# Performance work log

Hardware: AMD Instinct MI355X
Metric: run time of the kernel (lower is better)

## Reference

```python
import jax, jax.numpy as jnp
import numpy as np

B, S_IMG, S_TXT, H, D = 1, 2048, 512, 24, 128
HID = H * D  # 3072
S_TOT = S_TXT + S_IMG
IP_SCALE = 1.0
EPS = 1e-5


def setup_inputs() -> dict:
    key = jax.random.key(0)
    ks = jax.random.split(key, 16)
    r = lambda k, s: jax.random.normal(k, s, dtype=jnp.float32)
    w = lambda k, s: r(k, s) * 0.02
    theta = r(ks[15], (S_TOT, D))  # rotary angles over joint sequence
    z = lambda: jnp.zeros((HID,), jnp.float32)
    return dict(
        hidden_states=r(ks[0], (B, S_IMG, HID)),
        encoder_hidden_states=r(ks[1], (B, S_TXT, HID)),
        image_emb=r(ks[2], (B, 4, HID)),
        rope_cos=jnp.cos(theta), rope_sin=jnp.sin(theta),
        Wq=w(ks[3], (HID, HID)), bq=z(),
        Wk=w(ks[4], (HID, HID)), bk=z(),
        Wv=w(ks[5], (HID, HID)), bv=z(),
        Waq=w(ks[6], (HID, HID)), baq=z(),
        Wak=w(ks[7], (HID, HID)), bak=z(),
        Wav=w(ks[8], (HID, HID)), bav=z(),
        Wk_ip=w(ks[9], (HID, HID)),
        Wv_ip=w(ks[10], (HID, HID)),
        Wo=w(ks[11], (HID, HID)), bo=z(),
        Wao=w(ks[12], (HID, HID)), bao=z(),
    )


def _heads(x):  # [B,S,HID] -> [B,H,S,D]
    return x.reshape(x.shape[0], x.shape[1], H, D).transpose(0, 2, 1, 3)


def _unheads(x):  # [B,H,S,D] -> [B,S,HID]
    return x.transpose(0, 2, 1, 3).reshape(x.shape[0], x.shape[2], HID)


def _rmsnorm(x):  # over last dim, no affine (RMSNorm(128, affine=False))
    return x * jax.lax.rsqrt(jnp.mean(x * x, axis=-1, keepdims=True) + EPS)


def _rope(x, cos, sin):  # diffusers apply_rotary_emb, use_real, interleaved pairs
    xp = x.reshape(*x.shape[:-1], D // 2, 2)
    rot = jnp.stack([-xp[..., 1], xp[..., 0]], axis=-1).reshape(x.shape)
    return x * cos + rot * sin  # cos/sin [S,D] broadcast over [B,H,S,D]


def _sdpa(q, k, v):
    s = jnp.einsum('bhqd,bhkd->bhqk', q, k) / jnp.sqrt(jnp.asarray(D, q.dtype))
    return jnp.einsum('bhqk,bhkd->bhqd', jax.nn.softmax(s, axis=-1), v)


def _forward(hidden_states, encoder_hidden_states, image_emb, rope_cos, rope_sin,
             Wq, bq, Wk, bk, Wv, bv, Waq, baq, Wak, bak, Wav, bav,
             Wk_ip, Wv_ip, Wo, bo, Wao, bao):
    # main QKV over image-latent tokens
    q = _rmsnorm(_heads(hidden_states @ Wq.T + bq))
    k = _rmsnorm(_heads(hidden_states @ Wk.T + bk))
    v = _heads(hidden_states @ Wv.T + bv)
    # IP-adapter cross attention (query = latent q, kv from image_emb)
    k_ip = _rmsnorm(_heads(image_emb @ Wk_ip.T))
    v_ip = _heads(image_emb @ Wv_ip.T)
    ip_out = _unheads(_sdpa(q, k_ip, v_ip))  # [B,S_IMG,HID]
    # encoder (text) QKV, concat text-first as in Flux
    eq = _rmsnorm(_heads(encoder_hidden_states @ Waq.T + baq))
    ek = _rmsnorm(_heads(encoder_hidden_states @ Wak.T + bak))
    ev = _heads(encoder_hidden_states @ Wav.T + bav)
    q = jnp.concatenate([eq, q], axis=2)
    k = jnp.concatenate([ek, k], axis=2)
    v = jnp.concatenate([ev, v], axis=2)
    q = _rope(q, rope_cos, rope_sin)
    k = _rope(k, rope_cos, rope_sin)
    out = _unheads(_sdpa(q, k, v))  # [B,S_TOT,HID]
    enc_out, hid_out = out[:, :S_TXT], out[:, S_TXT:]
    hid_out = hid_out + IP_SCALE * ip_out
    hid_out = hid_out @ Wo.T + bo   # to_out[0] (+ identity dropout)
    enc_out = enc_out @ Wao.T + bao  # to_add_out
    return hid_out, enc_out


def reference(hidden_states, encoder_hidden_states, image_emb, rope_cos, rope_sin,
              Wq, bq, Wk, bk, Wv, bv, Waq, baq, Wak, bak, Wav, bav,
              Wk_ip, Wv_ip, Wo, bo, Wao, bao):
    return _forward(hidden_states, encoder_hidden_states, image_emb, rope_cos, rope_sin,
                    Wq, bq, Wk, bk, Wv, bv, Waq, baq, Wak, bak, Wav, bav,
                    Wk_ip, Wv_ip, Wo, bo, Wao, bao)
```

## Files before the change

### kernel.cpp

```cpp
#include <hip/hip_runtime.h>

typedef __bf16 bf16;
typedef __bf16 bf16x2 __attribute__((ext_vector_type(2)));
typedef __bf16 bf16x4 __attribute__((ext_vector_type(4)));
typedef __bf16 bf16x8 __attribute__((ext_vector_type(8)));
typedef float  f32x4  __attribute__((ext_vector_type(4)));

#define H_    24
#define D_    128
#define HID_  3072
#define SIMG_ 2048
#define STXT_ 512
#define STOT_ 2560
#define EPS_  1e-5f
#define SCALE_ 0.08838834764831845f
#define HH_   ((size_t)HID_*HID_)

typedef __attribute__((address_space(3))) unsigned int lds_uint;
typedef const __attribute__((address_space(1))) unsigned int glb_uint;
__device__ __forceinline__ void gll16(const void* g, void* l){
  __builtin_amdgcn_global_load_lds((glb_uint*)g, (lds_uint*)l, 16, 0, 0);
}

__device__ inline bf16x8 frag8f(const float* __restrict__ p){
  const f32x4 a = *(const f32x4*)p;
  const f32x4 b = *(const f32x4*)(p + 4);
  bf16x8 r;
  r[0]=(bf16)a[0]; r[1]=(bf16)a[1]; r[2]=(bf16)a[2]; r[3]=(bf16)a[3];
  r[4]=(bf16)b[0]; r[5]=(bf16)b[1]; r[6]=(bf16)b[2]; r[7]=(bf16)b[3];
  return r;
}

__global__ __launch_bounds__(256) void k_f2b(const float* __restrict__ src,
                                             bf16* __restrict__ dst, int n)
{
  const int i = ((int)blockIdx.x*256 + (int)threadIdx.x)*8;
  if (i + 7 < n){
    const f32x4 a = *(const f32x4*)(src + i);
    const f32x4 b = *(const f32x4*)(src + i + 4);
    bf16x8 o;
    o[0]=(bf16)a[0]; o[1]=(bf16)a[1]; o[2]=(bf16)a[2]; o[3]=(bf16)a[3];
    o[4]=(bf16)b[0]; o[5]=(bf16)b[1]; o[6]=(bf16)b[2]; o[7]=(bf16)b[3];
    *(bf16x8*)(dst + i) = o;
  }
}

__global__ __launch_bounds__(256) void k_f2bw8(
    const float* __restrict__ W0, const float* __restrict__ W1,
    const float* __restrict__ W2, const float* __restrict__ W3,
    const float* __restrict__ W4, const float* __restrict__ W5,
    const float* __restrict__ W6, const float* __restrict__ W7,
    bf16* __restrict__ out)
{
  const int wi = (int)blockIdx.y;
  const float* s = (wi==0)?W0:(wi==1)?W1:(wi==2)?W2:(wi==3)?W3:(wi==4)?W4:(wi==5)?W5:(wi==6)?W6:W7;
  bf16* d = out + (size_t)wi*HH_;
  const int i = ((int)blockIdx.x*256 + (int)threadIdx.x)*8;
  const f32x4 a = *(const f32x4*)(s + i);
  const f32x4 b = *(const f32x4*)(s + i + 4);
  bf16x8 o;
  o[0]=(bf16)a[0]; o[1]=(bf16)a[1]; o[2]=(bf16)a[2]; o[3]=(bf16)a[3];
  o[4]=(bf16)b[0]; o[5]=(bf16)b[1]; o[6]=(bf16)b[2]; o[7]=(bf16)b[3];
  *(bf16x8*)(d + i) = o;
}

#define MFMA_ __builtin_amdgcn_mfma_f32_16x16x32_bf16
#define MM(bfr, n) \
    acc[0][n]=MFMA_(af0,bfr,acc[0][n],0,0,0); acc[1][n]=MFMA_(af1,bfr,acc[1][n],0,0,0); \
    acc[2][n]=MFMA_(af2,bfr,acc[2][n],0,0,0); acc[3][n]=MFMA_(af3,bfr,acc[3][n],0,0,0);
#define WAIT6 asm volatile("s_waitcnt vmcnt(6)" ::: "memory")
#define WAIT0 asm volatile("s_waitcnt vmcnt(0)" ::: "memory")
#define NOWAIT (void)0

__device__ __forceinline__ void gemm8_core(
    const bf16* __restrict__ A, const bf16* __restrict__ W,
    int mb, int nb,
    f32x4 (&acc)[4][4],
    bf16 (&Al)[3][128][64],
    bf16 (&Bl)[3][256][64])
{
  const int t = (int)threadIdx.x;
  const int w = t >> 6, l = t & 63;
  const int lr = l & 15, lg = l >> 4;
  const int wr = w >> 2, wc = w & 3;
  const int srow = t >> 3;
  const int soff = ((t & 7) ^ (srow & 7)) * 8;

  const bf16* Abase = A + (size_t)(mb + srow)*HID_ + soff;
  const bf16* Wbase = W + (size_t)(nb + srow)*HID_ + soff;

#define SA(buf, tt, i) gll16(Abase + (size_t)(i)*64*HID_ + (tt)*64, &Al[buf][0][0] + (i)*4096 + t*8)
#define SB(buf, tt, i) gll16(Wbase + (size_t)(i)*64*HID_ + (tt)*64, &Bl[buf][0][0] + (i)*4096 + t*8)

  const int arow_ = wr*64 + lr;
  const int brow_ = wc*64 + lr;
  const int sx = lr & 7;

  SA(0,0,0); SA(0,0,1); SB(0,0,0); SB(0,0,1); SB(0,0,2); SB(0,0,3);
  SA(1,1,0); SA(1,1,1); SB(1,1,0); SB(1,1,1); SB(1,1,2); SB(1,1,3);
  WAIT6;
  __builtin_amdgcn_s_barrier();

#define TILE(C, NXT, TT, PRE, TW)                                            \
  {                                                                          \
    bf16x8 af0,af1,af2,af3,b0,b1;                                            \
    const int s0_ = (lg^sx)*8, s1_ = ((4+lg)^sx)*8;                          \
                                                        \
    af0=*(const bf16x8*)&Al[C][arow_   ][s0_];                               \
    af1=*(const bf16x8*)&Al[C][arow_+16][s0_];                               \
    af2=*(const bf16x8*)&Al[C][arow_+32][s0_];                               \
    af3=*(const bf16x8*)&Al[C][arow_+48][s0_];                               \
    b0 =*(const bf16x8*)&Bl[C][brow_   ][s0_];                               \
    b1 =*(const bf16x8*)&Bl[C][brow_+16][s0_];                               \
    if (PRE){ SA(NXT,(TT)+2,0); SA(NXT,(TT)+2,1); }                          \
    __builtin_amdgcn_s_setprio(1); MM(b0,0) MM(b1,1)                         \
    __builtin_amdgcn_s_setprio(0);                                           \
    __builtin_amdgcn_s_barrier();                                            \
                                                        \
    b0 =*(const bf16x8*)&Bl[C][brow_+32][s0_];                               \
    b1 =*(const bf16x8*)&Bl[C][brow_+48][s0_];                               \
    if (PRE){ SB(NXT,(TT)+2,0); SB(NXT,(TT)+2,1); }                          \
    __builtin_amdgcn_s_setprio(1); MM(b0,2) MM(b1,3)                         \
    __builtin_amdgcn_s_setprio(0);                                           \
    __builtin_amdgcn_s_barrier();                                            \
                                                        \
    af0=*(const bf16x8*)&Al[C][arow_   ][s1_];                               \
    af1=*(const bf16x8*)&Al[C][arow_+16][s1_];                               \
    af2=*(const bf16x8*)&Al[C][arow_+32][s1_];                               \
    af3=*(const bf16x8*)&Al[C][arow_+48][s1_];                               \
    b0 =*(const bf16x8*)&Bl[C][brow_   ][s1_];                               \
    b1 =*(const bf16x8*)&Bl[C][brow_+16][s1_];                               \
    if (PRE){ SB(NXT,(TT)+2,2); SB(NXT,(TT)+2,3); }                          \
    __builtin_amdgcn_s_setprio(1); MM(b0,0) MM(b1,1)                         \
    __builtin_amdgcn_s_setprio(0);                                           \
    __builtin_amdgcn_s_barrier();                                            \
                                                        \
    b0 =*(const bf16x8*)&Bl[C][brow_+32][s1_];                               \
    b1 =*(const bf16x8*)&Bl[C][brow_+48][s1_];                               \
    __builtin_amdgcn_s_setprio(1); MM(b0,2) MM(b1,3)                         \
    __builtin_amdgcn_s_setprio(0);                                           \
    TW;                                                                      \
    __builtin_amdgcn_s_barrier();                                            \
  }

  for (int base = 0; base < 45; base += 3){
    TILE(0, 2, base,   true, WAIT6);
    TILE(1, 0, base+1, true, WAIT6);
    TILE(2, 1, base+2, true, WAIT6);
  }
  TILE(0, 2, 45, true,  WAIT6);
  TILE(1, 0, 46, false, WAIT0);
  TILE(2, 1, 47, false, NOWAIT);
#undef TILE
#undef SA
#undef SB
}

__global__ __launch_bounds__(512, 1) void k_gemm8_qkv(
    const bf16* __restrict__ Ahid, const bf16* __restrict__ Aenc,
    const bf16* __restrict__ Wb,
    const float* bq, const float* bk, const float* bv,
    const float* baq, const float* bak, const float* bav,
    bf16* Cq, bf16* Ck, bf16* Cv, bf16* Ceq, bf16* Cek, bf16* Cev)
{
  __shared__ __align__(16) bf16 Al[3][128][64];
  __shared__ __align__(16) bf16 Bl[3][256][64];
  const int by = (int)blockIdx.y;
  const int enc = (by >= 16) ? 1 : 0;
  const int which = (int)blockIdx.x % 3;
  const int nb = ((int)blockIdx.x / 3)*256;
  const int mb = (enc ? (by - 16) : by)*128;
  const bf16* A = enc ? Aenc : Ahid;
  const int widx = which + enc*3;
  const bf16* W = Wb + (size_t)widx*HH_;
  const float* bias = (which==0) ? (enc?baq:bq) : (which==1) ? (enc?bak:bk) : (enc?bav:bv);
  bf16* Cm = (which==0) ? (enc?Ceq:Cq) : (which==1) ? (enc?Cek:Ck) : (enc?Cev:Cv);

  f32x4 acc[4][4] = {};
  gemm8_core(A, W, mb, nb, acc, Al, Bl);

  const int w = (int)(threadIdx.x >> 6), l = (int)(threadIdx.x & 63u);
  const int lr = l & 15, lg = l >> 4;
  const int wr = w >> 2, wc = w & 3;
  #pragma unroll
  for (int nf = 0; nf < 4; nf++){
    const int col = nb + wc*64 + nf*16 + lr;
    const float bvl = bias[col];
    #pragma unroll
    for (int m = 0; m < 4; m++){
      #pragma unroll
      for (int r = 0; r < 4; r++){
        const int row = mb + wr*64 + m*16 + lg*4 + r;
        Cm[(size_t)row*HID_ + col] = (bf16)(acc[m][nf][r] + bvl);
      }
    }
  }
}

__global__ __launch_bounds__(512, 1) void k_gemm8_out(
    const bf16* __restrict__ Ahid, const bf16* __restrict__ Aenc,
    const bf16* __restrict__ Wb,
    const float* bo, const float* bao, float* __restrict__ outp)
{
  __shared__ __align__(16) bf16 Al[3][128][64];
  __shared__ __align__(16) bf16 Bl[3][256][64];
  const int by = (int)blockIdx.y;
  const int enc = (by >= 16) ? 1 : 0;
  const int nb = (int)blockIdx.x*256;
  const int mb = (enc ? (by - 16) : by)*128;
  const bf16* A = enc ? Aenc : Ahid;
  const bf16* W = Wb + (size_t)(enc ? 7 : 6)*HH_;
  const float* bias = enc ? bao : bo;
  float* C = outp + (enc ? (size_t)SIMG_*HID_ : 0);

  f32x4 acc[4][4] = {};
  gemm8_core(A, W, mb, nb, acc, Al, Bl);

  const int w = (int)(threadIdx.x >> 6), l = (int)(threadIdx.x & 63u);
  const int lr = l & 15, lg = l >> 4;
  const int wr = w >> 2, wc = w & 3;
  #pragma unroll
  for (int nf = 0; nf < 4; nf++){
    const int col = nb + wc*64 + nf*16 + lr;
    const float bvl = bias[col];
    #pragma unroll
    for (int m = 0; m < 4; m++){
      #pragma unroll
      for (int r = 0; r < 4; r++){
        const int row = mb + wr*64 + m*16 + lg*4 + r;
        C[(size_t)row*HID_ + col] = acc[m][nf][r] + bvl;
      }
    }
  }
}

__global__ __launch_bounds__(256) void k_gemm_ip(const float* __restrict__ A,
    const float* __restrict__ Wk_, const float* __restrict__ Wv_,
    bf16* __restrict__ Ck_, bf16* __restrict__ Cv_)
{
  const float* Wm = blockIdx.y ? Wv_ : Wk_;
  bf16* C = blockIdx.y ? Cv_ : Ck_;
  const int w = (int)(threadIdx.x >> 6), l = (int)(threadIdx.x & 63u);
  const int lr = l & 15, lg = l >> 4;
  const int nbw = (int)blockIdx.x*64 + w*16;
  f32x4 acc = {};
  const float* arow = A + (size_t)((lr < 4) ? lr : 0)*HID_;
  const float* wrow = Wm + (size_t)(nbw + lr)*HID_;
  for (int k0 = 0; k0 < HID_; k0 += 32){
    const bf16x8 af  = frag8f(arow + k0 + lg*8);
    const bf16x8 bfr = frag8f(wrow + k0 + lg*8);
    acc = __builtin_amdgcn_mfma_f32_16x16x32_bf16(af, bfr, acc, 0, 0, 0);
  }
  if (lg == 0){
    #pragma unroll
    for (int r = 0; r < 4; r++)
      C[(size_t)r*HID_ + nbw + lr] = (bf16)acc[r];
  }
}

__global__ __launch_bounds__(256) void k_finish_qk(
    const bf16* __restrict__ rawQ, const bf16* __restrict__ rawK,
    const bf16* __restrict__ rawEQ, const bf16* __restrict__ rawEK,
    const float* __restrict__ cosT, const float* __restrict__ sinT,
    bf16* __restrict__ Qh, bf16* __restrict__ Kh)
{
  const int wid = (int)blockIdx.x*4 + (int)(threadIdx.x >> 6);
  const int l = (int)(threadIdx.x & 63u);
  const int s = wid / H_;
  const int h = wid % H_;
  const bf16 *sq_, *sk_;
  if (s < STXT_){
    const size_t off = (size_t)s*HID_ + h*D_;
    sq_ = rawEQ + off; sk_ = rawEK + off;
  } else {
    const size_t off = (size_t)(s - STXT_)*HID_ + h*D_;
    sq_ = rawQ + off; sk_ = rawK + off;
  }
  const int d0 = 2*l, d1 = 2*l + 1;
  float q0 = sq_[d0], q1 = sq_[d1];
  float k0 = sk_[d0], k1 = sk_[d1];
  float ssq = q0*q0 + q1*q1;
  float ssk = k0*k0 + k1*k1;
  #pragma unroll
  for (int m = 1; m < 64; m <<= 1){ ssq += __shfl_xor(ssq, m); ssk += __shfl_xor(ssk, m); }
  const float rq = rsqrtf(ssq*(1.0f/128.0f) + EPS_);
  const float rk = rsqrtf(ssk*(1.0f/128.0f) + EPS_);
  q0 *= rq; q1 *= rq; k0 *= rk; k1 *= rk;
  const float c0 = cosT[(size_t)s*D_ + d0], c1 = cosT[(size_t)s*D_ + d1];
  const float s0 = sinT[(size_t)s*D_ + d0], s1 = sinT[(size_t)s*D_ + d1];
  const float qo0 = q0*c0 - q1*s0, qo1 = q1*c1 + q0*s1;
  const float ko0 = k0*c0 - k1*s0, ko1 = k1*c1 + k0*s1;
  const size_t qoff = ((size_t)h*STOT_ + s)*D_ + d0;
  Qh[qoff] = (bf16)qo0; Qh[qoff + 1] = (bf16)qo1;
  Kh[qoff] = (bf16)ko0; Kh[qoff + 1] = (bf16)ko1;
}

__global__ __launch_bounds__(256) void k_vtrans(
    const bf16* __restrict__ rawV, const bf16* __restrict__ rawEV,
    bf16* __restrict__ Vt)
{
  __shared__ bf16 lt[128*130];
  const int t = (int)threadIdx.x;
  const int stile = (int)blockIdx.x*128;
  const int h = (int)blockIdx.y;
  #pragma unroll
  for (int i = 0; i < 8; i++){
    const int sl = i*16 + (t >> 4);
    const int s = stile + sl;
    const bf16* src = (s < STXT_) ? (rawEV + (size_t)s*HID_) : (rawV + (size_t)(s - STXT_)*HID_);
    const bf16x8 v = *(const bf16x8*)(src + h*D_ + (t & 15)*8);
    #pragma unroll
    for (int j = 0; j < 8; j++) lt[((t & 15)*8 + j)*130 + sl] = v[j];
  }
  __syncthreads();
  #pragma unroll
  for (int j = 0; j < 4; j++){
    const int d = j*32 + (t >> 3);
    const int s0 = (t & 7)*16;
    bf16x8 a, b;
    #pragma unroll
    for (int k = 0; k < 4; k++){
      const bf16x2 p = *(const bf16x2*)(lt + d*130 + s0 + 2*k);
      a[2*k] = p[0]; a[2*k+1] = p[1];
    }
    #pragma unroll
    for (int k = 0; k < 4; k++){
      const bf16x2 p = *(const bf16x2*)(lt + d*130 + s0 + 8 + 2*k);
      b[2*k] = p[0]; b[2*k+1] = p[1];
    }
    bf16* dst = Vt + ((size_t)h*D_ + d)*STOT_ + stile + s0;
    *(bf16x8*)dst = a;
    *(bf16x8*)(dst + 8) = b;
  }
}

__global__ __launch_bounds__(256) void k_finish_ip(
    const bf16* __restrict__ rawKip, const bf16* __restrict__ rawVip,
    float* __restrict__ Kip, float* __restrict__ Vip)
{
  const int wid = (int)blockIdx.x*4 + (int)(threadIdx.x >> 6);
  const int l = (int)(threadIdx.x & 63u);
  const int h = wid / 4, j = wid % 4;
  const int d0 = 2*l, d1 = 2*l + 1;
  const size_t src = (size_t)j*HID_ + h*D_;
  float k0 = rawKip[src + d0], k1 = rawKip[src + d1];
  float v0 = rawVip[src + d0], v1 = rawVip[src + d1];
  float ss = k0*k0 + k1*k1;
  #pragma unroll
  for (int m = 1; m < 64; m <<= 1) ss += __shfl_xor(ss, m);
  const float rk = rsqrtf(ss*(1.0f/128.0f) + EPS_);
  const size_t dst = ((size_t)h*4 + j)*D_;
  Kip[dst + d0] = k0*rk; Kip[dst + d1] = k1*rk;
  Vip[dst + d0] = v0;    Vip[dst + d1] = v1;
}

__global__ __launch_bounds__(256) void k_ip_attn(
    const bf16* __restrict__ rawQ, const float* __restrict__ Kip,
    const float* __restrict__ Vip, bf16* __restrict__ ipOut)
{
  const int wid = (int)blockIdx.x*4 + (int)(threadIdx.x >> 6);
  const int l = (int)(threadIdx.x & 63u);
  const int s = wid / H_, h = wid % H_;
  const int d0 = 2*l, d1 = 2*l + 1;
  const bf16* src = rawQ + (size_t)s*HID_ + h*D_;
  float q0 = src[d0], q1 = src[d1];
  float ss = q0*q0 + q1*q1;
  #pragma unroll
  for (int m = 1; m < 64; m <<= 1) ss += __shfl_xor(ss, m);
  const float r = rsqrtf(ss*(1.0f/128.0f) + EPS_);
  q0 *= r; q1 *= r;
  const float* kb = Kip + (size_t)h*4*D_;
  const float* vb = Vip + (size_t)h*4*D_;
  float sc[4];
  #pragma unroll
  for (int j = 0; j < 4; j++) sc[j] = q0*kb[j*D_ + d0] + q1*kb[j*D_ + d1];
  #pragma unroll
  for (int m = 1; m < 64; m <<= 1){
    #pragma unroll
    for (int j = 0; j < 4; j++) sc[j] += __shfl_xor(sc[j], m);
  }
  const float mx = fmaxf(fmaxf(sc[0], sc[1]), fmaxf(sc[2], sc[3]));
  float p[4], ps = 0.f;
  #pragma unroll
  for (int j = 0; j < 4; j++){ p[j] = __expf((sc[j] - mx)*SCALE_); ps += p[j]; }
  const float inv = 1.0f/ps;
  float o0 = 0.f, o1 = 0.f;
  #pragma unroll
  for (int j = 0; j < 4; j++){ o0 += p[j]*vb[j*D_ + d0]; o1 += p[j]*vb[j*D_ + d1]; }
  const size_t dst = (size_t)s*HID_ + h*D_;
  ipOut[dst + d0] = (bf16)(o0*inv);
  ipOut[dst + d1] = (bf16)(o1*inv);
}

__global__ __launch_bounds__(256, 2) void k_flash3(
    const bf16* __restrict__ Q, const bf16* __restrict__ K,
    const bf16* __restrict__ Vt, bf16* __restrict__ attnOut)
{
  __shared__ __align__(16) bf16 Ks[2][64*128];
  __shared__ __align__(16) bf16 Vs[2][128*64];
  __shared__ __align__(16) bf16 plds[4][32*64];
  const int t = (int)threadIdx.x;
  const int w = t >> 6, l = t & 63;
  const int lr = l & 15, lg = l >> 4;
  const int h = (int)blockIdx.x / 20;
  const int qbase = ((int)blockIdx.x % 20)*128 + w*32;
  const bf16* Qh = Q  + (size_t)h*STOT_*D_;
  const bf16* Kh = K  + (size_t)h*STOT_*D_;
  const bf16* Vh = Vt + (size_t)h*D_*STOT_;

  bf16x8 qf[2][4];
  #pragma unroll
  for (int qt = 0; qt < 2; qt++)
    #pragma unroll
    for (int kk = 0; kk < 4; kk++)
      qf[qt][kk] = *(const bf16x8*)(Qh + (size_t)(qbase + qt*16 + lr)*D_ + kk*32 + lg*8);

  f32x4 acc[2][8] = {};
  float mrun[2] = {-3.0e38f, -3.0e38f}, lrun[2] = {0.f, 0.f};

  const int krow = t >> 4, kslot = t & 15;
  const int vrow = t >> 3, vslot = t & 7;

  auto STAGE = [&](int buf, int kv){
    #pragma unroll
    for (int i = 0; i < 4; i++){
      const int r = i*16 + krow;
      gll16(Kh + (size_t)(kv + r)*D_ + ((kslot ^ (r & 7))*8),
            (void*)(&Ks[buf][0] + (size_t)t*8 + i*2048));
    }
    #pragma unroll
    for (int i = 0; i < 4; i++){
      const int r = i*32 + vrow;
      gll16(Vh + (size_t)r*STOT_ + kv + ((vslot ^ (r & 7))*8),
            (void*)(&Vs[buf][0] + (size_t)t*8 + i*2048));
    }
  };

  STAGE(0, 0);
  __syncthreads();
  int cur = 0;
  for (int kv = 0; kv < STOT_; kv += 64){
    if (kv + 64 < STOT_) STAGE(cur ^ 1, kv + 64);

    f32x4 st[2][4] = {};
    #pragma unroll
    for (int tt = 0; tt < 4; tt++){
      const int kr = tt*16 + lr;
      #pragma unroll
      for (int kk = 0; kk < 4; kk++){
        const bf16x8 kf = *(const bf16x8*)(&Ks[cur][0] + kr*128 + (((kk*4 + lg) ^ (kr & 7))*8));
        st[0][tt] = __builtin_amdgcn_mfma_f32_16x16x32_bf16(kf, qf[0][kk], st[0][tt], 0, 0, 0);
        st[1][tt] = __builtin_amdgcn_mfma_f32_16x16x32_bf16(kf, qf[1][kk], st[1][tt], 0, 0, 0);
      }
    }
    #pragma unroll
    for (int qt = 0; qt < 2; qt++){
      const int q = qt*16 + lr;
      float sv[4][4];
      float vmax = -3.0e38f;
      #pragma unroll
      for (int tt = 0; tt < 4; tt++)
        #pragma unroll
        for (int r = 0; r < 4; r++){ const float x = st[qt][tt][r]*SCALE_; sv[tt][r] = x; vmax = fmaxf(vmax, x); }
      vmax = fmaxf(vmax, __shfl_xor(vmax, 16));
      vmax = fmaxf(vmax, __shfl_xor(vmax, 32));
      const float mnew  = fmaxf(mrun[qt], vmax);
      const float alpha = __expf(mrun[qt] - mnew);
      float rs = 0.f;
      #pragma unroll
      for (int tt = 0; tt < 4; tt++){
        bf16x4 pq;
        #pragma unroll
        for (int r = 0; r < 4; r++){
          const float p = __expf(sv[tt][r] - mnew);
          rs += p;
          pq[r] = (bf16)p;
        }
        *(bf16x4*)(&plds[w][q*64 + (((tt*2 + (lg >> 1)) ^ (q & 7))*8) + (lg & 1)*4]) = pq;
      }
      rs += __shfl_xor(rs, 16);
      rs += __shfl_xor(rs, 32);
      lrun[qt] = lrun[qt]*alpha + rs;
      mrun[qt] = mnew;
      #pragma unroll
      for (int n = 0; n < 8; n++)
        #pragma unroll
        for (int r = 0; r < 4; r++) acc[qt][n][r] *= alpha;
    }
    #pragma unroll
    for (int ks = 0; ks < 2; ks++){
      const bf16x8 pb0 = *(const bf16x8*)(&plds[w][(lr)*64      + (((ks*4 + lg) ^ (lr & 7))*8)]);
      const bf16x8 pb1 = *(const bf16x8*)(&plds[w][(16 + lr)*64 + (((ks*4 + lg) ^ (lr & 7))*8)]);
      #pragma unroll
      for (int n = 0; n < 8; n++){
        const int vr = n*16 + lr;
        const bf16x8 vf = *(const bf16x8*)(&Vs[cur][0] + vr*64 + (((ks*4 + lg) ^ (vr & 7))*8));
        acc[0][n] = __builtin_amdgcn_mfma_f32_16x16x32_bf16(vf, pb0, acc[0][n], 0, 0, 0);
        acc[1][n] = __builtin_amdgcn_mfma_f32_16x16x32_bf16(vf, pb1, acc[1][n], 0, 0, 0);
      }
    }
    __syncthreads();
    cur ^= 1;
  }
  #pragma unroll
  for (int qt = 0; qt < 2; qt++){
    const float inv = 1.0f/lrun[qt];
    #pragma unroll
    for (int n = 0; n < 8; n++){
      #pragma unroll
      for (int r = 0; r < 4; r++){
        attnOut[(size_t)(qbase + qt*16 + lr)*HID_ + h*D_ + n*16 + lg*4 + r] = (bf16)(acc[qt][n][r]*inv);
      }
    }
  }
}

__global__ __launch_bounds__(256) void k_add_hid(
    const bf16* __restrict__ attn, const bf16* __restrict__ ip, bf16* __restrict__ outp)
{
  const size_t i = ((size_t)blockIdx.x*256 + threadIdx.x)*4;
  const bf16x4 a = *(const bf16x4*)(attn + (size_t)STXT_*HID_ + i);
  const bf16x4 b = *(const bf16x4*)(ip + i);
  bf16x4 o;
  #pragma unroll
  for (int c = 0; c < 4; c++) o[c] = (bf16)((float)a[c] + (float)b[c]);
  *(bf16x4*)(outp + i) = o;
}

extern "C" void kernel_launch(void* const* d_in, const int* in_sizes, int n_in,
                              void* d_out, int out_size, void* d_ws, size_t ws_size,
                              hipStream_t stream)
{
  const float* HS   = (const float*)d_in[0];
  const float* ENC  = (const float*)d_in[1];
  const float* IMG  = (const float*)d_in[2];
  const float* COS  = (const float*)d_in[3];
  const float* SIN  = (const float*)d_in[4];
  const float* Wq   = (const float*)d_in[5];  const float* bq  = (const float*)d_in[6];
  const float* Wk   = (const float*)d_in[7];  const float* bk  = (const float*)d_in[8];
  const float* Wv   = (const float*)d_in[9];  const float* bv  = (const float*)d_in[10];
  const float* Waq  = (const float*)d_in[11]; const float* baq = (const float*)d_in[12];
  const float* Wak  = (const float*)d_in[13]; const float* bak = (const float*)d_in[14];
  const float* Wav  = (const float*)d_in[15]; const float* bav = (const float*)d_in[16];
  const float* Wkip = (const float*)d_in[17]; const float* Wvip= (const float*)d_in[18];
  const float* Wo   = (const float*)d_in[19]; const float* bo  = (const float*)d_in[20];
  const float* Wao  = (const float*)d_in[21]; const float* bao = (const float*)d_in[22];

  char* wsb = (char*)d_ws;
  size_t off = 0;
  auto alloc = [&](size_t bytes) -> char* {
    char* p = wsb + off; off += (bytes + 255) & ~((size_t)255); return p;
  };
  bf16* rawQ   = (bf16*)alloc((size_t)SIMG_*HID_*2);
  bf16* rawK   = (bf16*)alloc((size_t)SIMG_*HID_*2);
  bf16* rawV   = (bf16*)alloc((size_t)SIMG_*HID_*2);
  bf16* rawEQ  = (bf16*)alloc((size_t)STXT_*HID_*2);
  bf16* rawEK  = (bf16*)alloc((size_t)STXT_*HID_*2);
  bf16* rawEV  = (bf16*)alloc((size_t)STXT_*HID_*2);
  bf16* rawKip = (bf16*)alloc((size_t)4*HID_*2);
  bf16* rawVip = (bf16*)alloc((size_t)4*HID_*2);
  bf16* Qb     = (bf16*)alloc((size_t)H_*STOT_*D_*2);
  bf16* Kb     = (bf16*)alloc((size_t)H_*STOT_*D_*2);
  bf16* Vtb    = (bf16*)alloc((size_t)H_*STOT_*D_*2);
  bf16* AOUT   = (bf16*)alloc((size_t)STOT_*HID_*2);
  bf16* IPOUT  = (bf16*)alloc((size_t)SIMG_*HID_*2);
  float* KIPF  = (float*)alloc((size_t)H_*4*D_*4);
  float* VIPF  = (float*)alloc((size_t)H_*4*D_*4);
  bf16* HSb    = (bf16*)alloc((size_t)SIMG_*HID_*2);
  bf16* ENCb   = (bf16*)alloc((size_t)STXT_*HID_*2);
  bf16* Wb8    = (bf16*)alloc((size_t)8*HH_*2);
  bf16* HIDIN  = HSb;

  dim3 blk(256);
  dim3 blk512(512);
  k_f2b<<<dim3(3072), blk, 0, stream>>>(HS,  HSb,  SIMG_*HID_);
  k_f2b<<<dim3(768),  blk, 0, stream>>>(ENC, ENCb, STXT_*HID_);
  k_f2bw8<<<dim3(4608,8), blk, 0, stream>>>(Wq, Wk, Wv, Waq, Wak, Wav, Wo, Wao, Wb8);
  k_gemm8_qkv<<<dim3(36,20), blk512, 0, stream>>>(HSb, ENCb, Wb8,
                                                  bq, bk, bv, baq, bak, bav,
                                                  rawQ, rawK, rawV, rawEQ, rawEK, rawEV);
  k_gemm_ip<<<dim3(48,2), blk, 0, stream>>>(IMG, Wkip, Wvip, rawKip, rawVip);
  k_finish_qk<<<dim3(15360), blk, 0, stream>>>(rawQ, rawK, rawEQ, rawEK, COS, SIN, Qb, Kb);
  k_vtrans<<<dim3(20,24), blk, 0, stream>>>(rawV, rawEV, Vtb);
  k_finish_ip<<<dim3(24), blk, 0, stream>>>(rawKip, rawVip, KIPF, VIPF);
  k_ip_attn<<<dim3(12288), blk, 0, stream>>>(rawQ, KIPF, VIPF, IPOUT);
  k_flash3<<<dim3(480), blk, 0, stream>>>(Qb, Kb, Vtb, AOUT);
  k_add_hid<<<dim3(6144), blk, 0, stream>>>(AOUT, IPOUT, HIDIN);
  float* outp = (float*)d_out;
  k_gemm8_out<<<dim3(12,20), blk512, 0, stream>>>(HIDIN, AOUT, Wb8, bo, bao, outp);
}
```

Baseline: 568.1 us.

## Cut GEMM intra-tile barriers and remap blocks for XCD-aware locality

Restructures the GEMM inner tile to load all A/B fragments for each k-half into registers up front. This drops three of the four per-tile workgroup barriers and lets MFMA run longer between syncs. It also remaps linear block ids so consecutive work items land on the same XCD (lin&7 striding) for the QKV, output GEMMs and flash attention, aiming for better L2 reuse of shared weight and K/V tiles. The costs are higher register pressure and looser synchronisation around the LDS triple buffer, which could introduce a hazard if a prefetch overwrites a buffer still being read.

```diff
diff --git a/kernel.cpp b/kernel.cpp
--- a/kernel.cpp
+++ b/kernel.cpp
@@ -65,9 +65,9 @@
 }
 
 #define MFMA_ __builtin_amdgcn_mfma_f32_16x16x32_bf16
-#define MM(bfr, n) \
-    acc[0][n]=MFMA_(af0,bfr,acc[0][n],0,0,0); acc[1][n]=MFMA_(af1,bfr,acc[1][n],0,0,0); \
-    acc[2][n]=MFMA_(af2,bfr,acc[2][n],0,0,0); acc[3][n]=MFMA_(af3,bfr,acc[3][n],0,0,0);
+#define MM4(x0,x1,x2,x3,bb,n) \
+    acc[0][n]=MFMA_(x0,bb,acc[0][n],0,0,0); acc[1][n]=MFMA_(x1,bb,acc[1][n],0,0,0); \
+    acc[2][n]=MFMA_(x2,bb,acc[2][n],0,0,0); acc[3][n]=MFMA_(x3,bb,acc[3][n],0,0,0);
 #define WAIT6 asm volatile("s_waitcnt vmcnt(6)" ::: "memory")
 #define WAIT0 asm volatile("s_waitcnt vmcnt(0)" ::: "memory")
 #define NOWAIT (void)0
@@ -103,41 +103,39 @@
 
 #define TILE(C, NXT, TT, PRE, TW)                                            \
   {                                                                          \
-    bf16x8 af0,af1,af2,af3,b0,b1;                                            \
     const int s0_ = (lg^sx)*8, s1_ = ((4+lg)^sx)*8;                          \
-                                                        \
-    af0=*(const bf16x8*)&Al[C][arow_   ][s0_];                               \
-    af1=*(const bf16x8*)&Al[C][arow_+16][s0_];                               \
-    af2=*(const bf16x8*)&Al[C][arow_+32][s0_];                               \
-    af3=*(const bf16x8*)&Al[C][arow_+48][s0_];                               \
-    b0 =*(const bf16x8*)&Bl[C][brow_   ][s0_];                               \
-    b1 =*(const bf16x8*)&Bl[C][brow_+16][s0_];                               \
+    bf16x8 a00,a01,a02,a03, a10,a11,a12,a13;                                 \
+    bf16x8 b00,b01,b02,b03, b10,b11,b12,b13;                                 \
+                                            \
+    a00=*(const bf16x8*)&Al[C][arow_   ][s0_];                               \
+    a01=*(const bf16x8*)&Al[C][arow_+16][s0_];                               \
+    a02=*(const bf16x8*)&Al[C][arow_+32][s0_];                               \
+    a03=*(const bf16x8*)&Al[C][arow_+48][s0_];                               \
+    b00=*(const bf16x8*)&Bl[C][brow_   ][s0_];                               \
+    b01=*(const bf16x8*)&Bl[C][brow_+16][s0_];                               \
+    b02=*(const bf16x8*)&Bl[C][brow_+32][s0_];                               \
+    b03=*(const bf16x8*)&Bl[C][brow_+48][s0_];                               \
     if (PRE){ SA(NXT,(TT)+2,0); SA(NXT,(TT)+2,1); }                          \
-    __builtin_amdgcn_s_setprio(1); MM(b0,0) MM(b1,1)                         \
+    __builtin_amdgcn_s_setprio(1);                                           \
+    MM4(a00,a01,a02,a03,b00,0) MM4(a00,a01,a02,a03,b01,1)                    \
     __builtin_amdgcn_s_setprio(0);                                           \
-    __builtin_amdgcn_s_barrier();                                            \
-                                                        \
-    b0 =*(const bf16x8*)&Bl[C][brow_+32][s0_];                               \
-    b1 =*(const bf16x8*)&Bl[C][brow_+48][s0_];                               \
+                   \
+    a10=*(const bf16x8*)&Al[C][arow_   ][s1_];                               \
+    a11=*(const bf16x8*)&Al[C][arow_+16][s1_];                               \
+    a12=*(const bf16x8*)&Al[C][arow_+32][s1_];                               \
+    a13=*(const bf16x8*)&Al[C][arow_+48][s1_];                               \
+    b10=*(const bf16x8*)&Bl[C][brow_   ][s1_];                               \
+    b11=*(const bf16x8*)&Bl[C][brow_+16][s1_];                               \
     if (PRE){ SB(NXT,(TT)+2,0); SB(NXT,(TT)+2,1); }                          \
-    __builtin_amdgcn_s_setprio(1); MM(b0,2) MM(b1,3)                         \
+    __builtin_amdgcn_s_setprio(1);                                           \
+    MM4(a00,a01,a02,a03,b02,2) MM4(a00,a01,a02,a03,b03,3)                    \
     __builtin_amdgcn_s_setprio(0);                                           \
-    __builtin_amdgcn_s_barrier();                                            \
-                                                        \
-    af0=*(const bf16x8*)&Al[C][arow_   ][s1_];                               \
-    af1=*(const bf16x8*)&Al[C][arow_+16][s1_];                               \
-    af2=*(const bf16x8*)&Al[C][arow_+32][s1_];                               \
-    af3=*(const bf16x8*)&Al[C][arow_+48][s1_];                               \
-    b0 =*(const bf16x8*)&Bl[C][brow_   ][s1_];                               \
-    b1 =*(const bf16x8*)&Bl[C][brow_+16][s1_];                               \
+    b12=*(const bf16x8*)&Bl[C][brow_+32][s1_];                               \
+    b13=*(const bf16x8*)&Bl[C][brow_+48][s1_];                               \
     if (PRE){ SB(NXT,(TT)+2,2); SB(NXT,(TT)+2,3); }                          \
-    __builtin_amdgcn_s_setprio(1); MM(b0,0) MM(b1,1)                         \
-    __builtin_amdgcn_s_setprio(0);                                           \
-    __builtin_amdgcn_s_barrier();                                            \
-                                                        \
-    b0 =*(const bf16x8*)&Bl[C][brow_+32][s1_];                               \
-    b1 =*(const bf16x8*)&Bl[C][brow_+48][s1_];                               \
-    __builtin_amdgcn_s_setprio(1); MM(b0,2) MM(b1,3)                         \
+    __builtin_amdgcn_s_setprio(1);                                           \
+    MM4(a10,a11,a12,a13,b10,0) MM4(a10,a11,a12,a13,b11,1)                    \
+    MM4(a10,a11,a12,a13,b12,2) MM4(a10,a11,a12,a13,b13,3)                    \
     __builtin_amdgcn_s_setprio(0);                                           \
     TW;                                                                      \
     __builtin_amdgcn_s_barrier();                                            \
@@ -165,11 +163,14 @@
 {
   __shared__ __align__(16) bf16 Al[3][128][64];
   __shared__ __align__(16) bf16 Bl[3][256][64];
-  const int by = (int)blockIdx.y;
-  const int enc = (by >= 16) ? 1 : 0;
-  const int which = (int)blockIdx.x % 3;
-  const int nb = ((int)blockIdx.x / 3)*256;
-  const int mb = (enc ? (by - 16) : by)*128;
+  const int lin = (int)blockIdx.x;
+  const int work = (lin & 7)*90 + (lin >> 3);
+  const int mt = work / 36;
+  const int ct = work % 36;
+  const int which = ct % 3;
+  const int nb = (ct/3)*256;
+  const int enc = (mt >= 16) ? 1 : 0;
+  const int mb = (enc ? (mt - 16) : mt)*128;
   const bf16* A = enc ? Aenc : Ahid;
   const int widx = which + enc*3;
   const bf16* W = Wb + (size_t)widx*HH_;
@@ -204,10 +205,12 @@
 {
   __shared__ __align__(16) bf16 Al[3][128][64];
   __shared__ __align__(16) bf16 Bl[3][256][64];
-  const int by = (int)blockIdx.y;
-  const int enc = (by >= 16) ? 1 : 0;
-  const int nb = (int)blockIdx.x*256;
-  const int mb = (enc ? (by - 16) : by)*128;
+  const int lin = (int)blockIdx.x;
+  const int work = (lin & 7)*30 + (lin >> 3);
+  const int mt = work / 12;
+  const int nb = (work % 12)*256;
+  const int enc = (mt >= 16) ? 1 : 0;
+  const int mb = (enc ? (mt - 16) : mt)*128;
   const bf16* A = enc ? Aenc : Ahid;
   const bf16* W = Wb + (size_t)(enc ? 7 : 6)*HH_;
   const float* bias = enc ? bao : bo;
@@ -402,8 +405,10 @@
   const int t = (int)threadIdx.x;
   const int w = t >> 6, l = t & 63;
   const int lr = l & 15, lg = l >> 4;
-  const int h = (int)blockIdx.x / 20;
-  const int qbase = ((int)blockIdx.x % 20)*128 + w*32;
+  const int lin = (int)blockIdx.x;
+  const int work = (lin & 7)*60 + (lin >> 3);
+  const int h = work / 20;
+  const int qbase = (work % 20)*128 + w*32;
   const bf16* Qh = Q  + (size_t)h*STOT_*D_;
   const bf16* Kh = K  + (size_t)h*STOT_*D_;
   const bf16* Vh = Vt + (size_t)h*D_*STOT_;
@@ -576,9 +581,9 @@
   k_f2b<<<dim3(3072), blk, 0, stream>>>(HS,  HSb,  SIMG_*HID_);
   k_f2b<<<dim3(768),  blk, 0, stream>>>(ENC, ENCb, STXT_*HID_);
   k_f2bw8<<<dim3(4608,8), blk, 0, stream>>>(Wq, Wk, Wv, Waq, Wak, Wav, Wo, Wao, Wb8);
-  k_gemm8_qkv<<<dim3(36,20), blk512, 0, stream>>>(HSb, ENCb, Wb8,
-                                                  bq, bk, bv, baq, bak, bav,
-                                                  rawQ, rawK, rawV, rawEQ, rawEK, rawEV);
+  k_gemm8_qkv<<<dim3(720), blk512, 0, stream>>>(HSb, ENCb, Wb8,
+                                                bq, bk, bv, baq, bak, bav,
+                                                rawQ, rawK, rawV, rawEQ, rawEK, rawEV);
   k_gemm_ip<<<dim3(48,2), blk, 0, stream>>>(IMG, Wkip, Wvip, rawKip, rawVip);
   k_finish_qk<<<dim3(15360), blk, 0, stream>>>(rawQ, rawK, rawEQ, rawEK, COS, SIN, Qb, Kb);
   k_vtrans<<<dim3(20,24), blk, 0, stream>>>(rawV, rawEV, Vtb);
@@ -587,5 +592,5 @@
   k_flash3<<<dim3(480), blk, 0, stream>>>(Qb, Kb, Vtb, AOUT);
   k_add_hid<<<dim3(6144), blk, 0, stream>>>(AOUT, IPOUT, HIDIN);
   float* outp = (float*)d_out;
-  k_gemm8_out<<<dim3(12,20), blk512, 0, stream>>>(HIDIN, AOUT, Wb8, bo, bao, outp);
-}
+  k_gemm8_out<<<dim3(240), blk512, 0, stream>>>(HIDIN, AOUT, Wb8, bo, bao, outp);
+}
```

Measured after the change: 565.0 us. Within noise of the previous version (-0.5%).

## Use 256x256 tiled QKV GEMM, trim GEMM barriers, XCD-aware block remapping

Applied to the files above, without the earlier changes.

Replaces the 128x256-tile QKV projection GEMM with a new 256x256-tile kernel. It uses a double-buffered LDS pipeline split into two K-halves and an 8x4 accumulator per wave, aiming to raise arithmetic intensity and reuse of each loaded tile. It also removes three intra-tile barriers from the shared GEMM core used by the output projection. The output-projection GEMM and the flash attention kernel get 1-D grids, with block indices remapped so neighbouring work lands on the same XCD for better L2 locality. Risks are higher register pressure from the larger accumulator and possible LDS hazards from the dropped barriers.

```diff
diff --git a/kernel.cpp b/kernel.cpp
--- a/kernel.cpp
+++ b/kernel.cpp
@@ -65,12 +65,134 @@
 }
 
 #define MFMA_ __builtin_amdgcn_mfma_f32_16x16x32_bf16
+#define WAITV4 asm volatile("s_waitcnt vmcnt(4)" ::: "memory")
+#define WAIT6  asm volatile("s_waitcnt vmcnt(6)" ::: "memory")
+#define WAIT0  asm volatile("s_waitcnt vmcnt(0)" ::: "memory")
+#define NOWAIT (void)0
+
+__global__ __launch_bounds__(512, 1) void k_gemm256_qkv(
+    const bf16* __restrict__ Ahid, const bf16* __restrict__ Aenc,
+    const bf16* __restrict__ Wb,
+    const float* bq, const float* bk, const float* bv,
+    const float* baq, const float* bak, const float* bav,
+    bf16* Cq, bf16* Ck, bf16* Cv, bf16* Ceq, bf16* Cek, bf16* Cev)
+{
+  __shared__ __align__(16) bf16 Abuf[2][2][128*64];
+  __shared__ __align__(16) bf16 Bbuf[2][2][128*64];
+  const int t = (int)threadIdx.x;
+  const int w = t >> 6, l = t & 63;
+  const int lr = l & 15, lg = l >> 4;
+  const int wr = w >> 2, wc = w & 3;
+  const int lin = (int)blockIdx.x;
+  const int which = lin % 3;
+  const int rest = lin / 3;
+  const int ntile = rest % 12;
+  const int mtile = rest / 12;
+  const int enc = (mtile >= 8) ? 1 : 0;
+  const int mb = (enc ? (mtile - 8) : mtile)*256;
+  const int nb = ntile*256;
+  const bf16* Ap = enc ? Aenc : Ahid;
+  const int widx = which + enc*3;
+  const bf16* Wp = Wb + (size_t)widx*HH_;
+  const float* bias = (which==0) ? (enc?baq:bq) : (which==1) ? (enc?bak:bk) : (enc?bav:bv);
+  bf16* Cm = (which==0) ? (enc?Ceq:Cq) : (which==1) ? (enc?Cek:Ck) : (enc?Cev:Cv);
+
+  const int line1 = t >> 3;
+  const int gu1 = (t & 7) ^ (line1 & 7);
+  const int row1 = 2*line1 + (gu1 >> 2);
+  const int s1 = gu1 & 3;
+  const bf16* Asrc = Ap + (size_t)(mb + row1)*HID_ + s1*8;
+  const bf16* Bsrc = Wp + (size_t)(nb + row1)*HID_ + s1*8;
+
+#define SH2(dbuf, j, TT) do{                                                   \
+    gll16(Asrc + (size_t)(TT)*64 + (j)*32, &Abuf[dbuf][j][0] + t*8);           \
+    gll16(Asrc + (size_t)128*HID_ + (size_t)(TT)*64 + (j)*32,                  \
+          &Abuf[dbuf][j][0] + 4096 + t*8);                                     \
+    gll16(Bsrc + (size_t)(TT)*64 + (j)*32, &Bbuf[dbuf][j][0] + t*8);           \
+    gll16(Bsrc + (size_t)128*HID_ + (size_t)(TT)*64 + (j)*32,                  \
+          &Bbuf[dbuf][j][0] + 4096 + t*8);                                     \
+  }while(0)
+
+  const int gx = ((((lr & 1) << 2) | lg) ^ ((lr >> 1) & 7)) * 8;
+  const int aoff0 = (wr*64 + 0*8 + (lr>>1))*64 + gx;
+  const int aoff1 = (wr*64 + 1*8 + (lr>>1))*64 + gx;
+  const int aoff2 = (wr*64 + 2*8 + (lr>>1))*64 + gx;
+  const int aoff3 = (wr*64 + 3*8 + (lr>>1))*64 + gx;
+  const int aoff4 = (wr*64 + 4*8 + (lr>>1))*64 + gx;
+  const int aoff5 = (wr*64 + 5*8 + (lr>>1))*64 + gx;
+  const int aoff6 = (wr*64 + 6*8 + (lr>>1))*64 + gx;
+  const int aoff7 = (wr*64 + 7*8 + (lr>>1))*64 + gx;
+  const int boff0 = (wc*32 + 0*8 + (lr>>1))*64 + gx;
+  const int boff1 = (wc*32 + 1*8 + (lr>>1))*64 + gx;
+  const int boff2 = (wc*32 + 2*8 + (lr>>1))*64 + gx;
+  const int boff3 = (wc*32 + 3*8 + (lr>>1))*64 + gx;
+
+  f32x4 acc[8][4] = {};
+
+#define MMROW(av, f) \
+  acc[f][0]=MFMA_(av,bb0,acc[f][0],0,0,0); acc[f][1]=MFMA_(av,bb1,acc[f][1],0,0,0); \
+  acc[f][2]=MFMA_(av,bb2,acc[f][2],0,0,0); acc[f][3]=MFMA_(av,bb3,acc[f][3],0,0,0);
+
+#define PHASE(cur, j, DO_PRE, TT, TW)                                          \
+  {                                                                            \
+    const bf16* __restrict__ Ah = &Abuf[cur][j][0];                            \
+    const bf16* __restrict__ Bh = &Bbuf[cur][j][0];                            \
+    bf16x8 bb0 = *(const bf16x8*)(Bh + boff0);                                 \
+    bf16x8 bb1 = *(const bf16x8*)(Bh + boff1);                                 \
+    bf16x8 bb2 = *(const bf16x8*)(Bh + boff2);                                 \
+    bf16x8 bb3 = *(const bf16x8*)(Bh + boff3);                                 \
+    bf16x8 aa0 = *(const bf16x8*)(Ah + aoff0);                                 \
+    bf16x8 aa1 = *(const bf16x8*)(Ah + aoff1);                                 \
+    bf16x8 aa2 = *(const bf16x8*)(Ah + aoff2);                                 \
+    bf16x8 aa3 = *(const bf16x8*)(Ah + aoff3);                                 \
+    if (DO_PRE) SH2((cur)^1, j, TT);                                           \
+    __builtin_amdgcn_s_setprio(1);                                             \
+    MMROW(aa0,0) MMROW(aa1,1) MMROW(aa2,2) MMROW(aa3,3)                        \
+    __builtin_amdgcn_s_setprio(0);                                             \
+    aa0 = *(const bf16x8*)(Ah + aoff4);                                        \
+    aa1 = *(const bf16x8*)(Ah + aoff5);                                        \
+    aa2 = *(const bf16x8*)(Ah + aoff6);                                        \
+    aa3 = *(const bf16x8*)(Ah + aoff7);                                        \
+    __builtin_amdgcn_s_setprio(1);                                             \
+    MMROW(aa0,4) MMROW(aa1,5) MMROW(aa2,6) MMROW(aa3,7)                        \
+    __builtin_amdgcn_s_setprio(0);                                             \
+    TW;                                                                        \
+    __builtin_amdgcn_s_barrier();                                              \
+  }
+
+  SH2(0, 0, 0); SH2(0, 1, 0);
+  WAITV4;
+  __builtin_amdgcn_s_barrier();
+
+  for (int tt = 0; tt < 47; ++tt){
+    const int cur = tt & 1;
+    PHASE(cur, 0, true, tt+1, WAITV4);
+    PHASE(cur, 1, true, tt+1, WAITV4);
+  }
+  PHASE(1, 0, false, 0, WAIT0);
+  PHASE(1, 1, false, 0, NOWAIT);
+#undef PHASE
+#undef MMROW
+#undef SH2
+
+  #pragma unroll
+  for (int n = 0; n < 4; n++){
+    const int col = nb + wc*64 + n*16 + lr;
+    const float bvl = bias[col];
+    #pragma unroll
+    for (int f = 0; f < 8; f++){
+      #pragma unroll
+      for (int r = 0; r < 4; r++){
+        const int row = mb + wr*128 + f*16 + lg*4 + r;
+        Cm[(size_t)row*HID_ + col] = (bf16)(acc[f][n][r] + bvl);
+      }
+    }
+  }
+}
+
 #define MM(bfr, n) \
     acc[0][n]=MFMA_(af0,bfr,acc[0][n],0,0,0); acc[1][n]=MFMA_(af1,bfr,acc[1][n],0,0,0); \
     acc[2][n]=MFMA_(af2,bfr,acc[2][n],0,0,0); acc[3][n]=MFMA_(af3,bfr,acc[3][n],0,0,0);
-#define WAIT6 asm volatile("s_waitcnt vmcnt(6)" ::: "memory")
-#define WAIT0 asm volatile("s_waitcnt vmcnt(0)" ::: "memory")
-#define NOWAIT (void)0
 
 __device__ __forceinline__ void gemm8_core(
     const bf16* __restrict__ A, const bf16* __restrict__ W,
@@ -103,9 +225,8 @@
 
 #define TILE(C, NXT, TT, PRE, TW)                                            \
   {                                                                          \
+    const int s0_ = (lg^sx)*8, s1_ = ((4+lg)^sx)*8;                          \
     bf16x8 af0,af1,af2,af3,b0,b1;                                            \
-    const int s0_ = (lg^sx)*8, s1_ = ((4+lg)^sx)*8;                          \
-                                                        \
     af0=*(const bf16x8*)&Al[C][arow_   ][s0_];                               \
     af1=*(const bf16x8*)&Al[C][arow_+16][s0_];                               \
     af2=*(const bf16x8*)&Al[C][arow_+32][s0_];                               \
@@ -115,15 +236,11 @@
     if (PRE){ SA(NXT,(TT)+2,0); SA(NXT,(TT)+2,1); }                          \
     __builtin_amdgcn_s_setprio(1); MM(b0,0) MM(b1,1)                         \
     __builtin_amdgcn_s_setprio(0);                                           \
-    __builtin_amdgcn_s_barrier();                                            \
-                                                        \
     b0 =*(const bf16x8*)&Bl[C][brow_+32][s0_];                               \
     b1 =*(const bf16x8*)&Bl[C][brow_+48][s0_];                               \
     if (PRE){ SB(NXT,(TT)+2,0); SB(NXT,(TT)+2,1); }                          \
     __builtin_amdgcn_s_setprio(1); MM(b0,2) MM(b1,3)                         \
     __builtin_amdgcn_s_setprio(0);                                           \
-    __builtin_amdgcn_s_barrier();                                            \
-                                                        \
     af0=*(const bf16x8*)&Al[C][arow_   ][s1_];                               \
     af1=*(const bf16x8*)&Al[C][arow_+16][s1_];                               \
     af2=*(const bf16x8*)&Al[C][arow_+32][s1_];                               \
@@ -133,8 +250,6 @@
     if (PRE){ SB(NXT,(TT)+2,2); SB(NXT,(TT)+2,3); }                          \
     __builtin_amdgcn_s_setprio(1); MM(b0,0) MM(b1,1)                         \
     __builtin_amdgcn_s_setprio(0);                                           \
-    __builtin_amdgcn_s_barrier();                                            \
-                                                        \
     b0 =*(const bf16x8*)&Bl[C][brow_+32][s1_];                               \
     b1 =*(const bf16x8*)&Bl[C][brow_+48][s1_];                               \
     __builtin_amdgcn_s_setprio(1); MM(b0,2) MM(b1,3)                         \
@@ -156,47 +271,6 @@
 #undef SB
 }
 
-__global__ __launch_bounds__(512, 1) void k_gemm8_qkv(
-    const bf16* __restrict__ Ahid, const bf16* __restrict__ Aenc,
-    const bf16* __restrict__ Wb,
-    const float* bq, const float* bk, const float* bv,
-    const float* baq, const float* bak, const float* bav,
-    bf16* Cq, bf16* Ck, bf16* Cv, bf16* Ceq, bf16* Cek, bf16* Cev)
-{
-  __shared__ __align__(16) bf16 Al[3][128][64];
-  __shared__ __align__(16) bf16 Bl[3][256][64];
-  const int by = (int)blockIdx.y;
-  const int enc = (by >= 16) ? 1 : 0;
-  const int which = (int)blockIdx.x % 3;
-  const int nb = ((int)blockIdx.x / 3)*256;
-  const int mb = (enc ? (by - 16) : by)*128;
-  const bf16* A = enc ? Aenc : Ahid;
-  const int widx = which + enc*3;
-  const bf16* W = Wb + (size_t)widx*HH_;
-  const float* bias = (which==0) ? (enc?baq:bq) : (which==1) ? (enc?bak:bk) : (enc?bav:bv);
-  bf16* Cm = (which==0) ? (enc?Ceq:Cq) : (which==1) ? (enc?Cek:Ck) : (enc?Cev:Cv);
-
-  f32x4 acc[4][4] = {};
-  gemm8_core(A, W, mb, nb, acc, Al, Bl);
-
-  const int w = (int)(threadIdx.x >> 6), l = (int)(threadIdx.x & 63u);
-  const int lr = l & 15, lg = l >> 4;
-  const int wr = w >> 2, wc = w & 3;
-  #pragma unroll
-  for (int nf = 0; nf < 4; nf++){
-    const int col = nb + wc*64 + nf*16 + lr;
-    const float bvl = bias[col];
-    #pragma unroll
-    for (int m = 0; m < 4; m++){
-      #pragma unroll
-      for (int r = 0; r < 4; r++){
-        const int row = mb + wr*64 + m*16 + lg*4 + r;
-        Cm[(size_t)row*HID_ + col] = (bf16)(acc[m][nf][r] + bvl);
-      }
-    }
-  }
-}
-
 __global__ __launch_bounds__(512, 1) void k_gemm8_out(
     const bf16* __restrict__ Ahid, const bf16* __restrict__ Aenc,
     const bf16* __restrict__ Wb,
@@ -204,10 +278,12 @@
 {
   __shared__ __align__(16) bf16 Al[3][128][64];
   __shared__ __align__(16) bf16 Bl[3][256][64];
-  const int by = (int)blockIdx.y;
-  const int enc = (by >= 16) ? 1 : 0;
-  const int nb = (int)blockIdx.x*256;
-  const int mb = (enc ? (by - 16) : by)*128;
+  const int lin = (int)blockIdx.x;
+  const int work = (lin & 7)*30 + (lin >> 3);
+  const int mt = work / 12;
+  const int nb = (work % 12)*256;
+  const int enc = (mt >= 16) ? 1 : 0;
+  const int mb = (enc ? (mt - 16) : mt)*128;
   const bf16* A = enc ? Aenc : Ahid;
   const bf16* W = Wb + (size_t)(enc ? 7 : 6)*HH_;
   const float* bias = enc ? bao : bo;
@@ -402,8 +478,10 @@
   const int t = (int)threadIdx.x;
   const int w = t >> 6, l = t & 63;
   const int lr = l & 15, lg = l >> 4;
-  const int h = (int)blockIdx.x / 20;
-  const int qbase = ((int)blockIdx.x % 20)*128 + w*32;
+  const int lin = (int)blockIdx.x;
+  const int work = (lin & 7)*60 + (lin >> 3);
+  const int h = work / 20;
+  const int qbase = (work % 20)*128 + w*32;
   const bf16* Qh = Q  + (size_t)h*STOT_*D_;
   const bf16* Kh = K  + (size_t)h*STOT_*D_;
   const bf16* Vh = Vt + (size_t)h*D_*STOT_;
@@ -576,7 +654,7 @@
   k_f2b<<<dim3(3072), blk, 0, stream>>>(HS,  HSb,  SIMG_*HID_);
   k_f2b<<<dim3(768),  blk, 0, stream>>>(ENC, ENCb, STXT_*HID_);
   k_f2bw8<<<dim3(4608,8), blk, 0, stream>>>(Wq, Wk, Wv, Waq, Wak, Wav, Wo, Wao, Wb8);
-  k_gemm8_qkv<<<dim3(36,20), blk512, 0, stream>>>(HSb, ENCb, Wb8,
+  k_gemm256_qkv<<<dim3(360), blk512, 0, stream>>>(HSb, ENCb, Wb8,
                                                   bq, bk, bv, baq, bak, bav,
                                                   rawQ, rawK, rawV, rawEQ, rawEK, rawEV);
   k_gemm_ip<<<dim3(48,2), blk, 0, stream>>>(IMG, Wkip, Wvip, rawKip, rawVip);
@@ -587,5 +665,5 @@
   k_flash3<<<dim3(480), blk, 0, stream>>>(Qb, Kb, Vtb, AOUT);
   k_add_hid<<<dim3(6144), blk, 0, stream>>>(AOUT, IPOUT, HIDIN);
   float* outp = (float*)d_out;
-  k_gemm8_out<<<dim3(12,20), blk512, 0, stream>>>(HIDIN, AOUT, Wb8, bo, bao, outp);
-}
+  k_gemm8_out<<<dim3(240), blk512, 0, stream>>>(HIDIN, AOUT, Wb8, bo, bao, outp);
+}
```

Measured after the change: 593.6 us. 4.5% more time.
